# Optimization experiments

Measured on AMD Instinct MI355X. Metric: run time of the kernel, lower is better.

Reference implementation:

```python
import jax, jax.numpy as jnp
import numpy as np

NUM_GRAPHS = 512


def setup_inputs() -> dict:
    key = jax.random.key(0)
    ks = jax.random.split(key, 12)
    N, E, D, H, C = 100000, 1600000, 128, 128, 10
    x = jax.random.normal(ks[0], (N, D), dtype=jnp.float32)
    edge_index = jax.random.randint(ks[1], (2, E), 0, N, dtype=jnp.int64)
    batch = jnp.sort(jax.random.randint(ks[2], (N,), 0, NUM_GRAPHS, dtype=jnp.int64))
    def glorot(k, fan_in, fan_out):
        s = jnp.sqrt(6.0 / (fan_in + fan_out))
        return jax.random.uniform(k, (fan_in, fan_out), jnp.float32, -s, s)
    return {
        "x": x, "edge_index": edge_index, "batch": batch,
        "W_init": glorot(ks[3], D, H), "b_init": jnp.zeros((H,), jnp.float32),
        "W_h0": glorot(ks[4], H, H), "b_h0": jnp.zeros((H,), jnp.float32),
        "W_h1": glorot(ks[5], H, H), "b_h1": jnp.zeros((H,), jnp.float32),
        "W_out": glorot(ks[6], H, C), "b_out": jnp.zeros((C,), jnp.float32),
    }


def reference(x, edge_index, batch, W_init, b_init, W_h0, b_h0, W_h1, b_h1, W_out, b_out):
    N = x.shape[0]
    loop = jnp.arange(N, dtype=edge_index.dtype)
    # add self-loops (PyG GCNConv default)
    row = jnp.concatenate([edge_index[0], loop])  # source
    col = jnp.concatenate([edge_index[1], loop])  # target
    # symmetric normalization D^-1/2 (A+I) D^-1/2, degrees on target index
    deg = jax.ops.segment_sum(jnp.ones_like(col, dtype=x.dtype), col, num_segments=N)
    dis = jnp.where(deg > 0, jax.lax.rsqrt(jnp.maximum(deg, 1e-12)), 0.0)
    norm = dis[row] * dis[col]  # [E+N]

    def gcn_conv(h, W, b):
        h = h @ W                                    # linear first (as in PyG)
        msg = h[row] * norm[:, None]                 # gather + scale
        return jax.ops.segment_sum(msg, col, num_segments=N) + b  # scatter-add

    h = jax.nn.relu(gcn_conv(x, W_init, b_init))
    h = jax.nn.relu(gcn_conv(h, W_h0, b_h0))
    h = jax.nn.relu(gcn_conv(h, W_h1, b_h1))
    h = gcn_conv(h, W_out, b_out)
    # global mean pooling over graphs
    sums = jax.ops.segment_sum(h, batch, num_segments=NUM_GRAPHS)
    cnt = jax.ops.segment_sum(jnp.ones((N, 1), h.dtype), batch, num_segments=NUM_GRAPHS)
    return sums / jnp.maximum(cnt, 1.0)
```

## Files before the change

kernel.cpp:

```cpp
#include <hip/hip_runtime.h>


#define SORTB 64

typedef unsigned short u16;
typedef unsigned int   u32;
typedef __attribute__((ext_vector_type(8))) short bf16x8;
typedef __attribute__((ext_vector_type(4))) float f32x4;

static __device__ __forceinline__ u16 f2bf(float x) {
    u32 u = __float_as_uint(x);
    u32 r = (u + 0x7fffu + ((u >> 16) & 1u)) >> 16;
    return (u16)r;
}
static __device__ __forceinline__ float bf_lo(u32 p) { return __uint_as_float(p << 16); }
static __device__ __forceinline__ float bf_hi(u32 p) { return __uint_as_float(p & 0xffff0000u); }

__global__ __launch_bounds__(256) void k_count(const int* __restrict__ col, int E,
                                               int* __restrict__ cnt,
                                               u16* __restrict__ rank) {
    int e = blockIdx.x * 256 + threadIdx.x;
    if (e < E) rank[e] = (u16)atomicAdd(&cnt[col[e]], 1);
}

__global__ __launch_bounds__(256) void k_lhist(const int* __restrict__ cnt, int N,
                                               int strip, int* __restrict__ blockhist) {
    __shared__ int h[256];
    int t = threadIdx.x, blk = blockIdx.x;
    h[t] = 0;
    __syncthreads();
    int s0 = blk * strip, s1 = min(s0 + strip, N);
    for (int i = s0 + t; i < s1; i += 256) atomicAdd(&h[min(cnt[i], 255)], 1);
    __syncthreads();
    blockhist[t * SORTB + blk] = h[t];
}

__global__ __launch_bounds__(1024) void k_scan2(int* __restrict__ tsum) {
    __shared__ int part[1024];
    int t = threadIdx.x;
    int base = t * 16;
    int local[16];
    int s = 0;
    #pragma unroll
    for (int i = 0; i < 16; ++i) { local[i] = tsum[base + i]; s += local[i]; }
    part[t] = s;
    __syncthreads();
    for (int off = 1; off < 1024; off <<= 1) {
        int v = part[t];
        int add = (t >= off) ? part[t - off] : 0;
        __syncthreads();
        part[t] = v + add;
        __syncthreads();
    }
    int run = (t == 0) ? 0 : part[t - 1];
    #pragma unroll
    for (int i = 0; i < 16; ++i) { int c = local[i]; tsum[base + i] = run; run += c; }
}

__global__ __launch_bounds__(256) void k_scatterR(const int* __restrict__ cnt, int N,
                                                  int strip,
                                                  const int* __restrict__ blockhist,
                                                  int* __restrict__ perm,
                                                  int* __restrict__ iperm,
                                                  int* __restrict__ rowptr,
                                                  int* __restrict__ csr,
                                                  float* __restrict__ dis) {
    __shared__ int pst[256], ebs[256], sc[256], boff[256];
    int t = threadIdx.x, blk = blockIdx.x;
    pst[t]  = blockhist[t * SORTB];
    boff[t] = blockhist[t * SORTB + blk];
    __syncthreads();
    int cntb = ((t == 255) ? N : pst[t + 1]) - pst[t];
    int contrib = cntb * ((t + 3) & ~3);
    sc[t] = contrib;
    __syncthreads();
    for (int off = 1; off < 256; off <<= 1) {
        int v = sc[t];
        int a = (t >= off) ? sc[t - off] : 0;
        __syncthreads();
        sc[t] = v + a;
        __syncthreads();
    }
    ebs[t] = (t == 0) ? 0 : sc[t - 1];
    if (blk == 0 && t == 255) rowptr[N] = sc[255];
    __syncthreads();
    int s0 = blk * strip, s1 = min(s0 + strip, N);
    for (int i = s0 + t; i < s1; i += 256) {
        int c = cnt[i];
        int b = min(c, 255);
        int pos = atomicAdd(&boff[b], 1);
        perm[pos] = i;
        iperm[i] = pos;
        int pad = (c + 3) & ~3;
        int rp = ebs[b] + (pos - pst[b]) * pad;
        rowptr[pos] = rp;
        for (int p = rp + c; p < rp + pad; ++p) csr[p] = N;
        dis[i] = rsqrtf((float)(c + 1));
    }
}

__global__ __launch_bounds__(256) void k_prep2(const float* __restrict__ W0,
                                               const float* __restrict__ W1,
                                               const float* __restrict__ W2,
                                               const float* __restrict__ Wo,
                                               u32* __restrict__ whi,
                                               u32* __restrict__ wlo, int C,
                                               const int* __restrict__ row,
                                               const int* __restrict__ col, int E,
                                               const int* __restrict__ rowptr,
                                               const int* __restrict__ iperm,
                                               const u16* __restrict__ rank,
                                               int* __restrict__ csr,
                                               const float* __restrict__ x,
                                               const float* __restrict__ dis,
                                               u16* __restrict__ bX,
                                               u16* __restrict__ bA,
                                               u16* __restrict__ bB,
                                               int N, int eb) {
    int bx = blockIdx.x;
    if (bx < 24) {
        int which = bx >> 3;
        const float* W = (which == 0) ? W0 : (which == 1) ? W1 : W2;
        int t = (bx & 7) * 256 + threadIdx.x;
        int lane = t & 63;
        int nk = t >> 6;
        int k0 = nk & 3;
        int ntile = nk >> 2;
        int n = ntile * 16 + (lane & 15);
        int kbase = k0 * 32 + (lane >> 4) * 8;
        u32 hi[4], lo[4];
        #pragma unroll
        for (int tt = 0; tt < 4; ++tt) {
            float w0 = W[(kbase + 2 * tt) * 128 + n];
            float w1 = W[(kbase + 2 * tt + 1) * 128 + n];
            u16 h0 = f2bf(w0), h1 = f2bf(w1);
            u16 l0 = f2bf(w0 - __uint_as_float((u32)h0 << 16));
            u16 l1 = f2bf(w1 - __uint_as_float((u32)h1 << 16));
            hi[tt] = (u32)h0 | ((u32)h1 << 16);
            lo[tt] = (u32)l0 | ((u32)l1 << 16);
        }
        uint4 qh = {hi[0], hi[1], hi[2], hi[3]};
        uint4 ql = {lo[0], lo[1], lo[2], lo[3]};
        int base = which * 2048;
        ((uint4*)whi)[base + t] = qh;
        ((uint4*)wlo)[base + t] = ql;
    } else if (bx == 24) {
        int t = threadIdx.x;
        int lane = t & 63;
        int k0 = t >> 6;
        int n = lane & 15;
        int kbase = k0 * 32 + (lane >> 4) * 8;
        bool vc = (n < C);
        u32 hi[4], lo[4];
        #pragma unroll
        for (int tt = 0; tt < 4; ++tt) {
            float w0 = vc ? Wo[(kbase + 2 * tt) * C + n] : 0.f;
            float w1 = vc ? Wo[(kbase + 2 * tt + 1) * C + n] : 0.f;
            u16 h0 = f2bf(w0), h1 = f2bf(w1);
            u16 l0 = f2bf(w0 - __uint_as_float((u32)h0 << 16));
            u16 l1 = f2bf(w1 - __uint_as_float((u32)h1 << 16));
            hi[tt] = (u32)h0 | ((u32)h1 << 16);
            lo[tt] = (u32)l0 | ((u32)l1 << 16);
        }
        uint4 qh = {hi[0], hi[1], hi[2], hi[3]};
        uint4 ql = {lo[0], lo[1], lo[2], lo[3]};
        ((uint4*)whi)[6144 + t] = qh;
        ((uint4*)wlo)[6144 + t] = ql;
    } else if (bx < 25 + eb) {
        int e = (bx - 25) * 256 + threadIdx.x;
        if (e < E) {
            int c = col[e];
            csr[rowptr[iperm[c]] + (int)rank[e]] = row[e];
        }
    } else {
        int i = (bx - 25 - eb) * 256 + threadIdx.x;
        int total = (N + 1) * 32;
        if (i >= total) return;
        int v = i >> 5;
        if (v < N) {
            float dv = dis[v];
            float4 val = ((const float4*)x)[i];
            ushort4 o;
            o.x = f2bf(dv * val.x); o.y = f2bf(dv * val.y);
            o.z = f2bf(dv * val.z); o.w = f2bf(dv * val.w);
            ((ushort4*)bX)[i] = o;
        } else {
            ushort4 z = {0, 0, 0, 0};
            ((ushort4*)bX)[i] = z;
            ((ushort4*)bA)[i] = z;
            ((ushort4*)bB)[i] = z;
        }
    }
}

__global__ __launch_bounds__(256) void k_fused(const u16* __restrict__ hin,
                                               const u32* __restrict__ whi,
                                               const u32* __restrict__ wlo,
                                               const float* __restrict__ bias,
                                               u16* __restrict__ hout,
                                               const int* __restrict__ rowptr,
                                               const int* __restrict__ csr,
                                               const float* __restrict__ dis,
                                               const int* __restrict__ perm,
                                               int N, int scale_out,
                                               int proj,
                                               const u32* __restrict__ pwhi,
                                               const u32* __restrict__ pwlo,
                                               u16* __restrict__ tmpC) {
    __shared__ u32 sS[32 * 68];
    __shared__ float dS[32];
    __shared__ int pS[32];
    int tid = threadIdx.x;
    int wave = tid >> 6;
    int lane = tid & 63;
    int row0 = ((int)gridDim.x - 1 - (int)blockIdx.x) * 32;
    const uint4* hin4 = (const uint4*)hin;

    int grp = lane >> 4;
    int sub = lane & 15;
    #pragma unroll
    for (int jj = 0; jj < 2; ++jj) {
        int rloc = wave * 8 + jj * 4 + grp;
        int p = row0 + rloc;
        bool hR = p < N;
        int ia = 0, rem = 0, r = N;
        float dv = 1.f;
        if (hR) {
            r   = perm[p];
            ia  = rowptr[p];
            rem = rowptr[p + 1] - ia;
            dv  = dis[r];
        }
        uint4 ps = hin4[((u32)r << 4) + sub];
        float a0 = bf_lo(ps.x), a1 = bf_hi(ps.x);
        float a2 = bf_lo(ps.y), a3 = bf_hi(ps.y);
        float a4 = bf_lo(ps.z), a5 = bf_hi(ps.z);
        float a6 = bf_lo(ps.w), a7 = bf_hi(ps.w);
        int m = rem;
        m = max(m, __shfl_xor(m, 16));
        m = max(m, __shfl_xor(m, 32));
        const int4* cq = (const int4*)(csr + ia);
        for (int k = 0; k < m; k += 8) {
            int4 q0 = cq[(k >> 2)];
            int4 q1 = cq[(k >> 2) + 1];
            bool v0 = k < rem;
            bool v1 = (k + 4) < rem;
            int n0 = v0 ? q0.x : N;
            int n1 = v0 ? q0.y : N;
            int n2 = v0 ? q0.z : N;
            int n3 = v0 ? q0.w : N;
            int n4 = v1 ? q1.x : N;
            int n5 = v1 ? q1.y : N;
            int n6 = v1 ? q1.z : N;
            int n7 = v1 ? q1.w : N;
            uint4 p0 = hin4[((u32)n0 << 4) + sub];
            uint4 p1 = hin4[((u32)n1 << 4) + sub];
            uint4 p2 = hin4[((u32)n2 << 4) + sub];
            uint4 p3 = hin4[((u32)n3 << 4) + sub];
            uint4 p4 = hin4[((u32)n4 << 4) + sub];
            uint4 p5 = hin4[((u32)n5 << 4) + sub];
            uint4 p6 = hin4[((u32)n6 << 4) + sub];
            uint4 p7 = hin4[((u32)n7 << 4) + sub];
            a0 += bf_lo(p0.x) + bf_lo(p1.x) + bf_lo(p2.x) + bf_lo(p3.x);
            a1 += bf_hi(p0.x) + bf_hi(p1.x) + bf_hi(p2.x) + bf_hi(p3.x);
            a2 += bf_lo(p0.y) + bf_lo(p1.y) + bf_lo(p2.y) + bf_lo(p3.y);
            a3 += bf_hi(p0.y) + bf_hi(p1.y) + bf_hi(p2.y) + bf_hi(p3.y);
            a4 += bf_lo(p0.z) + bf_lo(p1.z) + bf_lo(p2.z) + bf_lo(p3.z);
            a5 += bf_hi(p0.z) + bf_hi(p1.z) + bf_hi(p2.z) + bf_hi(p3.z);
            a6 += bf_lo(p0.w) + bf_lo(p1.w) + bf_lo(p2.w) + bf_lo(p3.w);
            a7 += bf_hi(p0.w) + bf_hi(p1.w) + bf_hi(p2.w) + bf_hi(p3.w);
            a0 += bf_lo(p4.x) + bf_lo(p5.x) + bf_lo(p6.x) + bf_lo(p7.x);
            a1 += bf_hi(p4.x) + bf_hi(p5.x) + bf_hi(p6.x) + bf_hi(p7.x);
            a2 += bf_lo(p4.y) + bf_lo(p5.y) + bf_lo(p6.y) + bf_lo(p7.y);
            a3 += bf_hi(p4.y) + bf_hi(p5.y) + bf_hi(p6.y) + bf_hi(p7.y);
            a4 += bf_lo(p4.z) + bf_lo(p5.z) + bf_lo(p6.z) + bf_lo(p7.z);
            a5 += bf_hi(p4.z) + bf_hi(p5.z) + bf_hi(p6.z) + bf_hi(p7.z);
            a6 += bf_lo(p4.w) + bf_lo(p5.w) + bf_lo(p6.w) + bf_lo(p7.w);
            a7 += bf_hi(p4.w) + bf_hi(p5.w) + bf_hi(p6.w) + bf_hi(p7.w);
        }
        u32 w0 = (u32)f2bf(dv * a0) | ((u32)f2bf(dv * a1) << 16);
        u32 w1 = (u32)f2bf(dv * a2) | ((u32)f2bf(dv * a3) << 16);
        u32 w2 = (u32)f2bf(dv * a4) | ((u32)f2bf(dv * a5) << 16);
        u32 w3 = (u32)f2bf(dv * a6) | ((u32)f2bf(dv * a7) << 16);
        sS[rloc * 65 + sub * 4 + 0] = w0;
        sS[rloc * 65 + sub * 4 + 1] = w1;
        sS[rloc * 65 + sub * 4 + 2] = w2;
        sS[rloc * 65 + sub * 4 + 3] = w3;
        if (sub == 0) { dS[rloc] = dv; pS[rloc] = r; }
    }
    __syncthreads();

    f32x4 acc[2][2] = {{{0.f,0.f,0.f,0.f},{0.f,0.f,0.f,0.f}},
                       {{0.f,0.f,0.f,0.f},{0.f,0.f,0.f,0.f}}};
    int mA = lane & 15;
    int qA = lane >> 4;
    #pragma unroll
    for (int k0 = 0; k0 < 4; ++k0) {
        union { u32 u[4]; bf16x8 v; } A0, A1;
        int ub = k0 * 16 + qA * 4;
        #pragma unroll
        for (int tt = 0; tt < 4; ++tt) {
            A0.u[tt] = sS[mA * 65 + ub + tt];
            A1.u[tt] = sS[(mA + 16) * 65 + ub + tt];
        }
        #pragma unroll
        for (int ct = 0; ct < 2; ++ct) {
            int ntk = ((2 * wave + ct) * 4 + k0) * 64 + lane;
            union { uint4 q; bf16x8 v; } BH, BL;
            BH.q = ((const uint4*)whi)[ntk];
            BL.q = ((const uint4*)wlo)[ntk];
            acc[0][ct] = __builtin_amdgcn_mfma_f32_16x16x32_bf16(A0.v, BH.v, acc[0][ct], 0, 0, 0);
            acc[0][ct] = __builtin_amdgcn_mfma_f32_16x16x32_bf16(A0.v, BL.v, acc[0][ct], 0, 0, 0);
            acc[1][ct] = __builtin_amdgcn_mfma_f32_16x16x32_bf16(A1.v, BH.v, acc[1][ct], 0, 0, 0);
            acc[1][ct] = __builtin_amdgcn_mfma_f32_16x16x32_bf16(A1.v, BL.v, acc[1][ct], 0, 0, 0);
        }
    }

    if (!proj) {
        #pragma unroll
        for (int rt = 0; rt < 2; ++rt) {
            #pragma unroll
            for (int ct = 0; ct < 2; ++ct) {
                int col = (2 * wave + ct) * 16 + (lane & 15);
                float bb = bias[col];
                #pragma unroll
                for (int r = 0; r < 4; ++r) {
                    int rloc = rt * 16 + (lane >> 4) * 4 + r;
                    if (row0 + rloc < N) {
                        int rr = pS[rloc];
                        float o = fmaxf(acc[rt][ct][r] + bb, 0.f);
                        if (scale_out) o *= dS[rloc];
                        hout[((u32)rr << 7) + col] = f2bf(o);
                    }
                }
            }
        }
    } else {
        __syncthreads();
        u16* hS16 = (u16*)sS;
        #pragma unroll
        for (int rt = 0; rt < 2; ++rt) {
            #pragma unroll
            for (int ct = 0; ct < 2; ++ct) {
                int col = (2 * wave + ct) * 16 + (lane & 15);
                float bb = bias[col];
                #pragma unroll
                for (int r = 0; r < 4; ++r) {
                    int rloc = rt * 16 + (lane >> 4) * 4 + r;
                    hS16[rloc * 136 + col] = f2bf(fmaxf(acc[rt][ct][r] + bb, 0.f));
                }
            }
        }
        __syncthreads();
        if (wave < 2) {
            int m2 = lane & 15;
            int quad = lane >> 4;
            f32x4 a2 = {0.f, 0.f, 0.f, 0.f};
            #pragma unroll
            for (int k0 = 0; k0 < 4; ++k0) {
                bf16x8 Afrag = *(bf16x8*)&hS16[(wave * 16 + m2) * 136 + k0 * 32 + quad * 8];
                union { uint4 q; bf16x8 v; } BH, BL;
                BH.q = ((const uint4*)pwhi)[k0 * 64 + lane];
                BL.q = ((const uint4*)pwlo)[k0 * 64 + lane];
                a2 = __builtin_amdgcn_mfma_f32_16x16x32_bf16(Afrag, BH.v, a2, 0, 0, 0);
                a2 = __builtin_amdgcn_mfma_f32_16x16x32_bf16(Afrag, BL.v, a2, 0, 0, 0);
            }
            #pragma unroll
            for (int r = 0; r < 4; ++r) {
                int rloc = wave * 16 + quad * 4 + r;
                if (row0 + rloc < N) {
                    int rr = pS[rloc];
                    tmpC[((u32)rr << 4) + m2] = f2bf(a2[r] * dS[rloc]);
                }
            }
        }
        if (blockIdx.x == 0 && tid < 16) tmpC[((u32)N << 4) + tid] = 0;
    }
}

__global__ __launch_bounds__(1024) void k_aggpool(const u16* __restrict__ tp,
                                                  const int* __restrict__ rowptr,
                                                  const int* __restrict__ csr,
                                                  const int* __restrict__ iperm,
                                                  const float* __restrict__ dis,
                                                  const int* __restrict__ batch,
                                                  const float* __restrict__ bout,
                                                  float* __restrict__ out,
                                                  int N, int C) {
    __shared__ float2 red[1024];
    int g = blockIdx.x;
    int tid = threadIdx.x;
    int c = tid & 7;
    int rg = tid >> 3;
    const u32* tp32 = (const u32*)tp;
    int lo = 0, hi = N;
    while (lo < hi) { int m = (lo + hi) >> 1; if (batch[m] < g) lo = m + 1; else hi = m; }
    int lb = lo;
    hi = N;
    while (lo < hi) { int m = (lo + hi) >> 1; if (batch[m] <= g) lo = m + 1; else hi = m; }
    int ub = lo;
    const int4* csr4 = (const int4*)csr;
    float px = 0.f, py = 0.f;
    for (int v = lb + rg; v < ub; v += 128) {
        u32 ps = tp32[((u32)v << 3) + c];
        float ax = bf_lo(ps), ay = bf_hi(ps);
        int pos = iperm[v];
        int i = rowptr[pos], e = rowptr[pos + 1];
        for (; i + 8 <= e; i += 8) {
            int4 q0 = csr4[(u32)i >> 2];
            int4 q1 = csr4[((u32)i >> 2) + 1];
            u32 p0 = tp32[((u32)q0.x << 3) + c];
            u32 p1 = tp32[((u32)q0.y << 3) + c];
            u32 p2 = tp32[((u32)q0.z << 3) + c];
            u32 p3 = tp32[((u32)q0.w << 3) + c];
            u32 p4 = tp32[((u32)q1.x << 3) + c];
            u32 p5 = tp32[((u32)q1.y << 3) + c];
            u32 p6 = tp32[((u32)q1.z << 3) + c];
            u32 p7 = tp32[((u32)q1.w << 3) + c];
            ax += bf_lo(p0) + bf_lo(p1) + bf_lo(p2) + bf_lo(p3)
                + bf_lo(p4) + bf_lo(p5) + bf_lo(p6) + bf_lo(p7);
            ay += bf_hi(p0) + bf_hi(p1) + bf_hi(p2) + bf_hi(p3)
                + bf_hi(p4) + bf_hi(p5) + bf_hi(p6) + bf_hi(p7);
        }
        if (i < e) {
            int4 q0 = csr4[(u32)i >> 2];
            u32 p0 = tp32[((u32)q0.x << 3) + c];
            u32 p1 = tp32[((u32)q0.y << 3) + c];
            u32 p2 = tp32[((u32)q0.z << 3) + c];
            u32 p3 = tp32[((u32)q0.w << 3) + c];
            ax += bf_lo(p0) + bf_lo(p1) + bf_lo(p2) + bf_lo(p3);
            ay += bf_hi(p0) + bf_hi(p1) + bf_hi(p2) + bf_hi(p3);
        }
        float dv = dis[v];
        px += dv * ax;
        py += dv * ay;
    }
    red[tid] = make_float2(px, py);
    __syncthreads();
    #pragma unroll
    for (int s = 64; s >= 1; s >>= 1) {
        if (rg < s) {
            float2 o = red[tid + s * 8];
            red[tid].x += o.x; red[tid].y += o.y;
        }
        __syncthreads();
    }
    if (tid < 8) {
        float cnt = (float)(ub - lb);
        float den = fmaxf(cnt, 1.0f);
        float2 s2 = red[tid];
        int ch0 = 2 * tid, ch1 = 2 * tid + 1;
        if (ch0 < C) out[g * C + ch0] = (s2.x + cnt * bout[ch0]) / den;
        if (ch1 < C) out[g * C + ch1] = (s2.y + cnt * bout[ch1]) / den;
    }
}

extern "C" void kernel_launch(void* const* d_in, const int* in_sizes, int n_in,
                              void* d_out, int out_size, void* d_ws, size_t ws_size,
                              hipStream_t stream) {
    const float* x      = (const float*)d_in[0];
    const int*   ei     = (const int*)d_in[1];
    const int*   batch  = (const int*)d_in[2];
    const float* W_init = (const float*)d_in[3];
    const float* b_init = (const float*)d_in[4];
    const float* W_h0   = (const float*)d_in[5];
    const float* b_h0   = (const float*)d_in[6];
    const float* W_h1   = (const float*)d_in[7];
    const float* b_h1   = (const float*)d_in[8];
    const float* W_out  = (const float*)d_in[9];
    const float* b_out  = (const float*)d_in[10];

    int N = in_sizes[0] / 128;
    int E = in_sizes[1] / 2;
    int C = in_sizes[10];
    int G = out_size / C;
    int strip = (N + SORTB - 1) / SORTB;

    size_t off = 0;
    auto alloc = [&](size_t bytes) -> char* {
        char* p = (char*)d_ws + off;
        off += (bytes + 255) & ~(size_t)255;
        return p;
    };
    u16*   bufX   = (u16*)  alloc((size_t)(N + 1) * 128 * 2);
    u16*   bufA   = (u16*)  alloc((size_t)(N + 1) * 128 * 2);
    u16*   bufB   = (u16*)  alloc((size_t)(N + 1) * 128 * 2);
    float* dis    = (float*)alloc((size_t)N * 4);
    int*   rowptr = (int*)  alloc((size_t)(N + 1) * 4);
    int*   csr    = (int*)  alloc(((size_t)E + 3 * (size_t)N + 8) * 4);
    u32*   whi    = (u32*)  alloc((3 * 2048 + 256) * 16);
    u32*   wlo    = (u32*)  alloc((3 * 2048 + 256) * 16);
    int*   perm   = (int*)  alloc((size_t)N * 4);
    int*   iperm  = (int*)  alloc((size_t)N * 4);
    int*   blockhist = (int*)alloc((size_t)256 * SORTB * 4);
    size_t zoff   = off;
    int*   cnt    = (int*)  alloc((size_t)N * 4);
    size_t zbytes = off - zoff;

    u16*   rank   = (u16*)bufB;
    u16*   tmpC   = (u16*)bufX;

    hipMemsetAsync(cnt, 0, zbytes, stream);

    const int* rowi = ei;
    const int* coli = ei + E;

    int eb = (E + 255) / 256;
    int cg = ((N + 1) * 32 + 255) / 256;
    k_count<<<eb, 256, 0, stream>>>(coli, E, cnt, rank);
    k_lhist<<<SORTB, 256, 0, stream>>>(cnt, N, strip, blockhist);
    k_scan2<<<1, 1024, 0, stream>>>(blockhist);
    k_scatterR<<<SORTB, 256, 0, stream>>>(cnt, N, strip, blockhist, perm, iperm, rowptr, csr, dis);
    k_prep2<<<25 + eb + cg, 256, 0, stream>>>(W_init, W_h0, W_h1, W_out, whi, wlo, C,
                                              rowi, coli, E, rowptr, iperm, rank, csr,
                                              x, dis, bufX, bufA, bufB, N, eb);

    int fb = (N + 31) / 32;

    k_fused<<<fb, 256, 0, stream>>>(bufX, whi,         wlo,         b_init, bufA, rowptr, csr, dis, perm, N, 1, 0, nullptr, nullptr, nullptr);
    k_fused<<<fb, 256, 0, stream>>>(bufA, whi + 8192,  wlo + 8192,  b_h0,   bufB, rowptr, csr, dis, perm, N, 1, 0, nullptr, nullptr, nullptr);
    k_fused<<<fb, 256, 0, stream>>>(bufB, whi + 16384, wlo + 16384, b_h1,   bufA, rowptr, csr, dis, perm, N, 0, 1, whi + 24576, wlo + 24576, tmpC);

    k_aggpool<<<G, 1024, 0, stream>>>(tmpC, rowptr, csr, iperm, dis, batch, b_out, (float*)d_out, N, C);
}
```

Before: 441.1 us.

## Merge three GCN layer kernels into one cooperative persistent kernel; fold scan into scatter

Replaces the three per-layer k_fused launches with a single cooperative persistent kernel that loops over tiles and uses grid-wide syncs between layers, falling back to separate launches if the cooperative launch fails. It also removes the separate k_scan2 launch by having each k_scatterR block recompute the histogram prefix sums itself. The aim is to cut kernel launch and tail overhead. In exchange it pays for grid-sync cost, lower parallelism per tile loop, possible occupancy limits from the cooperative grid size, and redundant per-block histogram scanning.

```diff
diff --git a/kernel.cpp b/kernel.cpp
--- a/kernel.cpp
+++ b/kernel.cpp
@@ -1,4 +1,5 @@
 #include <hip/hip_runtime.h>
+#include <hip/hip_cooperative_groups.h>
 
 
 #define SORTB 64
@@ -33,28 +34,6 @@
     for (int i = s0 + t; i < s1; i += 256) atomicAdd(&h[min(cnt[i], 255)], 1);
     __syncthreads();
     blockhist[t * SORTB + blk] = h[t];
-}
-
-__global__ __launch_bounds__(1024) void k_scan2(int* __restrict__ tsum) {
-    __shared__ int part[1024];
-    int t = threadIdx.x;
-    int base = t * 16;
-    int local[16];
-    int s = 0;
-    #pragma unroll
-    for (int i = 0; i < 16; ++i) { local[i] = tsum[base + i]; s += local[i]; }
-    part[t] = s;
-    __syncthreads();
-    for (int off = 1; off < 1024; off <<= 1) {
-        int v = part[t];
-        int add = (t >= off) ? part[t - off] : 0;
-        __syncthreads();
-        part[t] = v + add;
-        __syncthreads();
-    }
-    int run = (t == 0) ? 0 : part[t - 1];
-    #pragma unroll
-    for (int i = 0; i < 16; ++i) { int c = local[i]; tsum[base + i] = run; run += c; }
 }
 
 __global__ __launch_bounds__(256) void k_scatterR(const int* __restrict__ cnt, int N,
@@ -67,12 +46,26 @@
                                                   float* __restrict__ dis) {
     __shared__ int pst[256], ebs[256], sc[256], boff[256];
     int t = threadIdx.x, blk = blockIdx.x;
-    pst[t]  = blockhist[t * SORTB];
-    boff[t] = blockhist[t * SORTB + blk];
-    __syncthreads();
-    int cntb = ((t == 255) ? N : pst[t + 1]) - pst[t];
-    int contrib = cntb * ((t + 3) & ~3);
-    sc[t] = contrib;
+    const int* rowp = blockhist + t * SORTB;
+    int rowSum = 0, before = 0;
+    for (int k = 0; k < SORTB; ++k) {
+        int v = rowp[k];
+        rowSum += v;
+        if (k < blk) before += v;
+    }
+    sc[t] = rowSum;
+    __syncthreads();
+    for (int off = 1; off < 256; off <<= 1) {
+        int v = sc[t];
+        int a = (t >= off) ? sc[t - off] : 0;
+        __syncthreads();
+        sc[t] = v + a;
+        __syncthreads();
+    }
+    pst[t] = (t == 0) ? 0 : sc[t - 1];
+    boff[t] = pst[t] + before;
+    __syncthreads();
+    sc[t] = rowSum * ((t + 3) & ~3);
     __syncthreads();
     for (int off = 1; off < 256; off <<= 1) {
         int v = sc[t];
@@ -193,27 +186,14 @@
     }
 }
 
-__global__ __launch_bounds__(256) void k_fused(const u16* __restrict__ hin,
-                                               const u32* __restrict__ whi,
-                                               const u32* __restrict__ wlo,
-                                               const float* __restrict__ bias,
-                                               u16* __restrict__ hout,
-                                               const int* __restrict__ rowptr,
-                                               const int* __restrict__ csr,
-                                               const float* __restrict__ dis,
-                                               const int* __restrict__ perm,
-                                               int N, int scale_out,
-                                               int proj,
-                                               const u32* __restrict__ pwhi,
-                                               const u32* __restrict__ pwlo,
-                                               u16* __restrict__ tmpC) {
-    __shared__ u32 sS[32 * 68];
-    __shared__ float dS[32];
-    __shared__ int pS[32];
-    int tid = threadIdx.x;
-    int wave = tid >> 6;
-    int lane = tid & 63;
-    int row0 = ((int)gridDim.x - 1 - (int)blockIdx.x) * 32;
+static __device__ __forceinline__ void tile_body(
+    int row0, const u16* hin, const u32* wh, const u32* wl,
+    const float* __restrict__ bias, u16* hout,
+    const int* __restrict__ rowptr, const int* __restrict__ csr,
+    const float* __restrict__ dis, const int* __restrict__ perm,
+    int N, int scale_out, int proj,
+    const u32* pwhi, const u32* pwlo, u16* tmpC,
+    u32* sS, float* dS, int* pS, int tid, int wave, int lane) {
     const uint4* hin4 = (const uint4*)hin;
 
     int grp = lane >> 4;
@@ -307,8 +287,8 @@
         for (int ct = 0; ct < 2; ++ct) {
             int ntk = ((2 * wave + ct) * 4 + k0) * 64 + lane;
             union { uint4 q; bf16x8 v; } BH, BL;
-            BH.q = ((const uint4*)whi)[ntk];
-            BL.q = ((const uint4*)wlo)[ntk];
+            BH.q = ((const uint4*)wh)[ntk];
+            BL.q = ((const uint4*)wl)[ntk];
             acc[0][ct] = __builtin_amdgcn_mfma_f32_16x16x32_bf16(A0.v, BH.v, acc[0][ct], 0, 0, 0);
             acc[0][ct] = __builtin_amdgcn_mfma_f32_16x16x32_bf16(A0.v, BL.v, acc[0][ct], 0, 0, 0);
             acc[1][ct] = __builtin_amdgcn_mfma_f32_16x16x32_bf16(A1.v, BH.v, acc[1][ct], 0, 0, 0);
@@ -376,6 +356,58 @@
         }
         if (blockIdx.x == 0 && tid < 16) tmpC[((u32)N << 4) + tid] = 0;
     }
+}
+
+__global__ __launch_bounds__(256) void k_fusedAll(
+        const u16* bX, u16* bA, u16* bB,
+        const u32* __restrict__ whi, const u32* __restrict__ wlo,
+        const float* __restrict__ bi0, const float* __restrict__ bi1,
+        const float* __restrict__ bi2,
+        const int* __restrict__ rowptr, const int* __restrict__ csr,
+        const float* __restrict__ dis, const int* __restrict__ perm,
+        int N, int fb, u16* tmpC) {
+    cooperative_groups::grid_group gg = cooperative_groups::this_grid();
+    __shared__ u32 sS[32 * 68];
+    __shared__ float dS[32];
+    __shared__ int pS[32];
+    int tid = threadIdx.x, wave = tid >> 6, lane = tid & 63;
+    for (int layer = 0; layer < 3; ++layer) {
+        const u16* hin = (layer == 0) ? bX : (layer == 1) ? bA : bB;
+        u16* hout = (layer == 0) ? bA : bB;
+        const u32* wh = whi + layer * 8192;
+        const u32* wl = wlo + layer * 8192;
+        const float* bias = (layer == 0) ? bi0 : (layer == 1) ? bi1 : bi2;
+        int proj = (layer == 2) ? 1 : 0;
+        for (int p = blockIdx.x; p < fb; p += gridDim.x) {
+            int row0 = (fb - 1 - p) * 32;
+            tile_body(row0, hin, wh, wl, bias, hout, rowptr, csr, dis, perm,
+                      N, proj ? 0 : 1, proj, whi + 24576, wlo + 24576, tmpC,
+                      sS, dS, pS, tid, wave, lane);
+            __syncthreads();
+        }
+        if (layer < 2) gg.sync();
+    }
+}
+
+__global__ __launch_bounds__(256) void k_fused(const u16* hin,
+                                               const u32* __restrict__ whi,
+                                               const u32* __restrict__ wlo,
+                                               const float* __restrict__ bias,
+                                               u16* hout,
+                                               const int* __restrict__ rowptr,
+                                               const int* __restrict__ csr,
+                                               const float* __restrict__ dis,
+                                               const int* __restrict__ perm,
+                                               int N, int scale_out, int proj,
+                                               const u32* pwhi, const u32* pwlo,
+                                               u16* tmpC) {
+    __shared__ u32 sS[32 * 68];
+    __shared__ float dS[32];
+    __shared__ int pS[32];
+    int tid = threadIdx.x, wave = tid >> 6, lane = tid & 63;
+    int row0 = ((int)gridDim.x - 1 - (int)blockIdx.x) * 32;
+    tile_body(row0, hin, whi, wlo, bias, hout, rowptr, csr, dis, perm,
+              N, scale_out, proj, pwhi, pwlo, tmpC, sS, dS, pS, tid, wave, lane);
 }
 
 __global__ __launch_bounds__(1024) void k_aggpool(const u16* __restrict__ tp,
@@ -509,7 +541,6 @@
     int cg = ((N + 1) * 32 + 255) / 256;
     k_count<<<eb, 256, 0, stream>>>(coli, E, cnt, rank);
     k_lhist<<<SORTB, 256, 0, stream>>>(cnt, N, strip, blockhist);
-    k_scan2<<<1, 1024, 0, stream>>>(blockhist);
     k_scatterR<<<SORTB, 256, 0, stream>>>(cnt, N, strip, blockhist, perm, iperm, rowptr, csr, dis);
     k_prep2<<<25 + eb + cg, 256, 0, stream>>>(W_init, W_h0, W_h1, W_out, whi, wlo, C,
                                               rowi, coli, E, rowptr, iperm, rank, csr,
@@ -517,9 +548,34 @@
 
     int fb = (N + 31) / 32;
 
-    k_fused<<<fb, 256, 0, stream>>>(bufX, whi,         wlo,         b_init, bufA, rowptr, csr, dis, perm, N, 1, 0, nullptr, nullptr, nullptr);
-    k_fused<<<fb, 256, 0, stream>>>(bufA, whi + 8192,  wlo + 8192,  b_h0,   bufB, rowptr, csr, dis, perm, N, 1, 0, nullptr, nullptr, nullptr);
-    k_fused<<<fb, 256, 0, stream>>>(bufB, whi + 16384, wlo + 16384, b_h1,   bufA, rowptr, csr, dis, perm, N, 0, 1, whi + 24576, wlo + 24576, tmpC);
+    bool coop_ok = false;
+    int maxB = 0;
+    if (hipOccupancyMaxActiveBlocksPerMultiprocessor(&maxB, k_fusedAll, 256, 0)
+            == hipSuccess && maxB > 0) {
+        static int numCU = 0;
+        if (numCU == 0) {
+            hipDeviceProp_t prop;
+            if (hipGetDeviceProperties(&prop, 0) == hipSuccess)
+                numCU = prop.multiProcessorCount;
+            if (numCU <= 0) numCU = 256;
+        }
+        int grid = maxB * numCU;
+        if (grid > fb) grid = fb;
+        void* kargs[] = { (void*)&bufX, (void*)&bufA, (void*)&bufB,
+                          (void*)&whi, (void*)&wlo,
+                          (void*)&b_init, (void*)&b_h0, (void*)&b_h1,
+                          (void*)&rowptr, (void*)&csr, (void*)&dis, (void*)&perm,
+                          (void*)&N, (void*)&fb, (void*)&tmpC };
+        hipError_t err = hipLaunchCooperativeKernel((const void*)k_fusedAll,
+                                                    dim3(grid), dim3(256),
+                                                    kargs, 0, stream);
+        coop_ok = (err == hipSuccess);
+    }
+    if (!coop_ok) {
+        k_fused<<<fb, 256, 0, stream>>>(bufX, whi,         wlo,         b_init, bufA, rowptr, csr, dis, perm, N, 1, 0, nullptr, nullptr, nullptr);
+        k_fused<<<fb, 256, 0, stream>>>(bufA, whi + 8192,  wlo + 8192,  b_h0,   bufB, rowptr, csr, dis, perm, N, 1, 0, nullptr, nullptr, nullptr);
+        k_fused<<<fb, 256, 0, stream>>>(bufB, whi + 16384, wlo + 16384, b_h1,   bufA, rowptr, csr, dis, perm, N, 0, 1, whi + 24576, wlo + 24576, tmpC);
+    }
 
     k_aggpool<<<G, 1024, 0, stream>>>(tmpC, rowptr, csr, iperm, dis, batch, b_out, (float*)d_out, N, C);
 }
```

New measurement: 652.5 us. 1.48x slower.

## Merge graph preprocessing kernels into one cooperative kernel with grid syncs

Applied to the files above, without the earlier changes.

Replaces the memset plus count, histogram, scan, scatter and prep kernels with a single cooperative kernel that uses grid-wide syncs between phases. The separate scan kernel goes away: each scatter block now sums its own histogram row directly. The intent is to remove several kernel launch gaps and tiny serial kernels. In exchange, the grid is capped at occupancy, so the large per-edge and per-node phases loop over work with grid-stride, and each grid sync adds a barrier cost. The previous multi-kernel path is kept as a fallback if the cooperative launch fails.

```diff
diff --git a/kernel.cpp b/kernel.cpp
--- a/kernel.cpp
+++ b/kernel.cpp
@@ -1,4 +1,5 @@
 #include <hip/hip_runtime.h>
+#include <hip/hip_cooperative_groups.h>
 
 
 #define SORTB 64
@@ -16,63 +17,50 @@
 static __device__ __forceinline__ float bf_lo(u32 p) { return __uint_as_float(p << 16); }
 static __device__ __forceinline__ float bf_hi(u32 p) { return __uint_as_float(p & 0xffff0000u); }
 
-__global__ __launch_bounds__(256) void k_count(const int* __restrict__ col, int E,
-                                               int* __restrict__ cnt,
-                                               u16* __restrict__ rank) {
-    int e = blockIdx.x * 256 + threadIdx.x;
-    if (e < E) rank[e] = (u16)atomicAdd(&cnt[col[e]], 1);
-}
-
-__global__ __launch_bounds__(256) void k_lhist(const int* __restrict__ cnt, int N,
-                                               int strip, int* __restrict__ blockhist) {
-    __shared__ int h[256];
-    int t = threadIdx.x, blk = blockIdx.x;
+
+static __device__ __forceinline__ void lhist_body(int blk, const int* __restrict__ cnt,
+                                                  int N, int strip,
+                                                  int* __restrict__ blockhist,
+                                                  int* h, int t) {
     h[t] = 0;
     __syncthreads();
     int s0 = blk * strip, s1 = min(s0 + strip, N);
     for (int i = s0 + t; i < s1; i += 256) atomicAdd(&h[min(cnt[i], 255)], 1);
     __syncthreads();
     blockhist[t * SORTB + blk] = h[t];
-}
-
-__global__ __launch_bounds__(1024) void k_scan2(int* __restrict__ tsum) {
-    __shared__ int part[1024];
-    int t = threadIdx.x;
-    int base = t * 16;
-    int local[16];
-    int s = 0;
-    #pragma unroll
-    for (int i = 0; i < 16; ++i) { local[i] = tsum[base + i]; s += local[i]; }
-    part[t] = s;
-    __syncthreads();
-    for (int off = 1; off < 1024; off <<= 1) {
-        int v = part[t];
-        int add = (t >= off) ? part[t - off] : 0;
+    __syncthreads();
+}
+
+static __device__ __forceinline__ void scatter_body(int blk, const int* __restrict__ cnt,
+                                                    int N, int strip,
+                                                    const int* __restrict__ blockhist,
+                                                    int* __restrict__ perm,
+                                                    int* __restrict__ iperm,
+                                                    int* __restrict__ rowptr,
+                                                    int* __restrict__ csr,
+                                                    float* __restrict__ dis,
+                                                    int* pst, int* ebs, int* sc, int* boff,
+                                                    int t) {
+    const int* rowp = blockhist + t * SORTB;
+    int rowSum = 0, before = 0;
+    for (int k = 0; k < SORTB; ++k) {
+        int v = rowp[k];
+        rowSum += v;
+        if (k < blk) before += v;
+    }
+    sc[t] = rowSum;
+    __syncthreads();
+    for (int off = 1; off < 256; off <<= 1) {
+        int v = sc[t];
+        int a = (t >= off) ? sc[t - off] : 0;
         __syncthreads();
-        part[t] = v + add;
+        sc[t] = v + a;
         __syncthreads();
     }
-    int run = (t == 0) ? 0 : part[t - 1];
-    #pragma unroll
-    for (int i = 0; i < 16; ++i) { int c = local[i]; tsum[base + i] = run; run += c; }
-}
-
-__global__ __launch_bounds__(256) void k_scatterR(const int* __restrict__ cnt, int N,
-                                                  int strip,
-                                                  const int* __restrict__ blockhist,
-                                                  int* __restrict__ perm,
-                                                  int* __restrict__ iperm,
-                                                  int* __restrict__ rowptr,
-                                                  int* __restrict__ csr,
-                                                  float* __restrict__ dis) {
-    __shared__ int pst[256], ebs[256], sc[256], boff[256];
-    int t = threadIdx.x, blk = blockIdx.x;
-    pst[t]  = blockhist[t * SORTB];
-    boff[t] = blockhist[t * SORTB + blk];
-    __syncthreads();
-    int cntb = ((t == 255) ? N : pst[t + 1]) - pst[t];
-    int contrib = cntb * ((t + 3) & ~3);
-    sc[t] = contrib;
+    pst[t] = (t == 0) ? 0 : sc[t - 1];
+    boff[t] = pst[t] + before;
+    __syncthreads();
+    sc[t] = rowSum * ((t + 3) & ~3);
     __syncthreads();
     for (int off = 1; off < 256; off <<= 1) {
         int v = sc[t];
@@ -97,6 +85,150 @@
         for (int p = rp + c; p < rp + pad; ++p) csr[p] = N;
         dis[i] = rsqrtf((float)(c + 1));
     }
+}
+
+static __device__ __forceinline__ void prep_unit(int u, int t,
+        const float* __restrict__ W0, const float* __restrict__ W1,
+        const float* __restrict__ W2, const float* __restrict__ Wo,
+        u32* __restrict__ whi, u32* __restrict__ wlo, int C,
+        const int* __restrict__ row, const int* __restrict__ col, int E,
+        const int* __restrict__ rowptr, const int* __restrict__ iperm,
+        const u16* __restrict__ rank, int* __restrict__ csr,
+        const float* __restrict__ x, const float* __restrict__ dis,
+        u16* __restrict__ bX, u16* __restrict__ bA, u16* __restrict__ bB,
+        int N, int eb) {
+    if (u < 24) {
+        int which = u >> 3;
+        const float* W = (which == 0) ? W0 : (which == 1) ? W1 : W2;
+        int t2 = (u & 7) * 256 + t;
+        int lane = t2 & 63;
+        int nk = t2 >> 6;
+        int k0 = nk & 3;
+        int ntile = nk >> 2;
+        int n = ntile * 16 + (lane & 15);
+        int kbase = k0 * 32 + (lane >> 4) * 8;
+        u32 hi[4], lo[4];
+        #pragma unroll
+        for (int tt = 0; tt < 4; ++tt) {
+            float w0 = W[(kbase + 2 * tt) * 128 + n];
+            float w1 = W[(kbase + 2 * tt + 1) * 128 + n];
+            u16 h0 = f2bf(w0), h1 = f2bf(w1);
+            u16 l0 = f2bf(w0 - __uint_as_float((u32)h0 << 16));
+            u16 l1 = f2bf(w1 - __uint_as_float((u32)h1 << 16));
+            hi[tt] = (u32)h0 | ((u32)h1 << 16);
+            lo[tt] = (u32)l0 | ((u32)l1 << 16);
+        }
+        uint4 qh = {hi[0], hi[1], hi[2], hi[3]};
+        uint4 ql = {lo[0], lo[1], lo[2], lo[3]};
+        int base = which * 2048;
+        ((uint4*)whi)[base + t2] = qh;
+        ((uint4*)wlo)[base + t2] = ql;
+    } else if (u == 24) {
+        int lane = t & 63;
+        int k0 = t >> 6;
+        int n = lane & 15;
+        int kbase = k0 * 32 + (lane >> 4) * 8;
+        bool vc = (n < C);
+        u32 hi[4], lo[4];
+        #pragma unroll
+        for (int tt = 0; tt < 4; ++tt) {
+            float w0 = vc ? Wo[(kbase + 2 * tt) * C + n] : 0.f;
+            float w1 = vc ? Wo[(kbase + 2 * tt + 1) * C + n] : 0.f;
+            u16 h0 = f2bf(w0), h1 = f2bf(w1);
+            u16 l0 = f2bf(w0 - __uint_as_float((u32)h0 << 16));
+            u16 l1 = f2bf(w1 - __uint_as_float((u32)h1 << 16));
+            hi[tt] = (u32)h0 | ((u32)h1 << 16);
+            lo[tt] = (u32)l0 | ((u32)l1 << 16);
+        }
+        uint4 qh = {hi[0], hi[1], hi[2], hi[3]};
+        uint4 ql = {lo[0], lo[1], lo[2], lo[3]};
+        ((uint4*)whi)[6144 + t] = qh;
+        ((uint4*)wlo)[6144 + t] = ql;
+    } else if (u < 25 + eb) {
+        int e = (u - 25) * 256 + t;
+        if (e < E) {
+            int c = col[e];
+            csr[rowptr[iperm[c]] + (int)rank[e]] = row[e];
+        }
+    } else {
+        int i = (u - 25 - eb) * 256 + t;
+        int total = (N + 1) * 32;
+        if (i < total) {
+            int v = i >> 5;
+            if (v < N) {
+                float dv = dis[v];
+                float4 val = ((const float4*)x)[i];
+                ushort4 o;
+                o.x = f2bf(dv * val.x); o.y = f2bf(dv * val.y);
+                o.z = f2bf(dv * val.z); o.w = f2bf(dv * val.w);
+                ((ushort4*)bX)[i] = o;
+            } else {
+                ushort4 z = {0, 0, 0, 0};
+                ((ushort4*)bX)[i] = z;
+                ((ushort4*)bA)[i] = z;
+                ((ushort4*)bB)[i] = z;
+            }
+        }
+    }
+}
+
+__global__ __launch_bounds__(256) void k_prepAll(
+        const int* __restrict__ rowi, const int* __restrict__ coli,
+        int E, int N, int strip,
+        int* __restrict__ cnt, u16* __restrict__ rank,
+        int* __restrict__ blockhist,
+        int* __restrict__ perm, int* __restrict__ iperm,
+        int* __restrict__ rowptr, int* __restrict__ csr,
+        float* __restrict__ dis,
+        const float* __restrict__ W0, const float* __restrict__ W1,
+        const float* __restrict__ W2, const float* __restrict__ Wo,
+        u32* __restrict__ whi, u32* __restrict__ wlo, int C,
+        const float* __restrict__ x,
+        u16* __restrict__ bX, u16* __restrict__ bA, u16* __restrict__ bB,
+        int eb, int cg) {
+    cooperative_groups::grid_group gg = cooperative_groups::this_grid();
+    __shared__ int pst[256], ebs[256], sc[256], boff[256];
+    int t = threadIdx.x, bx = blockIdx.x, G = gridDim.x;
+    for (int i = bx * 256 + t; i < N; i += G * 256) cnt[i] = 0;
+    gg.sync();
+    for (int e = bx * 256 + t; e < E; e += G * 256)
+        rank[e] = (u16)atomicAdd(&cnt[coli[e]], 1);
+    gg.sync();
+    if (bx < SORTB) lhist_body(bx, cnt, N, strip, blockhist, sc, t);
+    gg.sync();
+    if (bx < SORTB) scatter_body(bx, cnt, N, strip, blockhist, perm, iperm,
+                                 rowptr, csr, dis, pst, ebs, sc, boff, t);
+    gg.sync();
+    int total_u = 25 + eb + cg;
+    for (int u = bx; u < total_u; u += G)
+        prep_unit(u, t, W0, W1, W2, Wo, whi, wlo, C, rowi, coli, E,
+                  rowptr, iperm, rank, csr, x, dis, bX, bA, bB, N, eb);
+}
+
+__global__ __launch_bounds__(256) void k_count(const int* __restrict__ col, int E,
+                                               int* __restrict__ cnt,
+                                               u16* __restrict__ rank) {
+    int e = blockIdx.x * 256 + threadIdx.x;
+    if (e < E) rank[e] = (u16)atomicAdd(&cnt[col[e]], 1);
+}
+
+__global__ __launch_bounds__(256) void k_lhist(const int* __restrict__ cnt, int N,
+                                               int strip, int* __restrict__ blockhist) {
+    __shared__ int h[256];
+    lhist_body(blockIdx.x, cnt, N, strip, blockhist, h, threadIdx.x);
+}
+
+__global__ __launch_bounds__(256) void k_scatterR(const int* __restrict__ cnt, int N,
+                                                  int strip,
+                                                  const int* __restrict__ blockhist,
+                                                  int* __restrict__ perm,
+                                                  int* __restrict__ iperm,
+                                                  int* __restrict__ rowptr,
+                                                  int* __restrict__ csr,
+                                                  float* __restrict__ dis) {
+    __shared__ int pst[256], ebs[256], sc[256], boff[256];
+    scatter_body(blockIdx.x, cnt, N, strip, blockhist, perm, iperm,
+                 rowptr, csr, dis, pst, ebs, sc, boff, threadIdx.x);
 }
 
 __global__ __launch_bounds__(256) void k_prep2(const float* __restrict__ W0,
@@ -117,80 +249,8 @@
                                                u16* __restrict__ bA,
                                                u16* __restrict__ bB,
                                                int N, int eb) {
-    int bx = blockIdx.x;
-    if (bx < 24) {
-        int which = bx >> 3;
-        const float* W = (which == 0) ? W0 : (which == 1) ? W1 : W2;
-        int t = (bx & 7) * 256 + threadIdx.x;
-        int lane = t & 63;
-        int nk = t >> 6;
-        int k0 = nk & 3;
-        int ntile = nk >> 2;
-        int n = ntile * 16 + (lane & 15);
-        int kbase = k0 * 32 + (lane >> 4) * 8;
-        u32 hi[4], lo[4];
-        #pragma unroll
-        for (int tt = 0; tt < 4; ++tt) {
-            float w0 = W[(kbase + 2 * tt) * 128 + n];
-            float w1 = W[(kbase + 2 * tt + 1) * 128 + n];
-            u16 h0 = f2bf(w0), h1 = f2bf(w1);
-            u16 l0 = f2bf(w0 - __uint_as_float((u32)h0 << 16));
-            u16 l1 = f2bf(w1 - __uint_as_float((u32)h1 << 16));
-            hi[tt] = (u32)h0 | ((u32)h1 << 16);
-            lo[tt] = (u32)l0 | ((u32)l1 << 16);
-        }
-        uint4 qh = {hi[0], hi[1], hi[2], hi[3]};
-        uint4 ql = {lo[0], lo[1], lo[2], lo[3]};
-        int base = which * 2048;
-        ((uint4*)whi)[base + t] = qh;
-        ((uint4*)wlo)[base + t] = ql;
-    } else if (bx == 24) {
-        int t = threadIdx.x;
-        int lane = t & 63;
-        int k0 = t >> 6;
-        int n = lane & 15;
-        int kbase = k0 * 32 + (lane >> 4) * 8;
-        bool vc = (n < C);
-        u32 hi[4], lo[4];
-        #pragma unroll
-        for (int tt = 0; tt < 4; ++tt) {
-            float w0 = vc ? Wo[(kbase + 2 * tt) * C + n] : 0.f;
-            float w1 = vc ? Wo[(kbase + 2 * tt + 1) * C + n] : 0.f;
-            u16 h0 = f2bf(w0), h1 = f2bf(w1);
-            u16 l0 = f2bf(w0 - __uint_as_float((u32)h0 << 16));
-            u16 l1 = f2bf(w1 - __uint_as_float((u32)h1 << 16));
-            hi[tt] = (u32)h0 | ((u32)h1 << 16);
-            lo[tt] = (u32)l0 | ((u32)l1 << 16);
-        }
-        uint4 qh = {hi[0], hi[1], hi[2], hi[3]};
-        uint4 ql = {lo[0], lo[1], lo[2], lo[3]};
-        ((uint4*)whi)[6144 + t] = qh;
-        ((uint4*)wlo)[6144 + t] = ql;
-    } else if (bx < 25 + eb) {
-        int e = (bx - 25) * 256 + threadIdx.x;
-        if (e < E) {
-            int c = col[e];
-            csr[rowptr[iperm[c]] + (int)rank[e]] = row[e];
-        }
-    } else {
-        int i = (bx - 25 - eb) * 256 + threadIdx.x;
-        int total = (N + 1) * 32;
-        if (i >= total) return;
-        int v = i >> 5;
-        if (v < N) {
-            float dv = dis[v];
-            float4 val = ((const float4*)x)[i];
-            ushort4 o;
-            o.x = f2bf(dv * val.x); o.y = f2bf(dv * val.y);
-            o.z = f2bf(dv * val.z); o.w = f2bf(dv * val.w);
-            ((ushort4*)bX)[i] = o;
-        } else {
-            ushort4 z = {0, 0, 0, 0};
-            ((ushort4*)bX)[i] = z;
-            ((ushort4*)bA)[i] = z;
-            ((ushort4*)bB)[i] = z;
-        }
-    }
+    prep_unit(blockIdx.x, threadIdx.x, W0, W1, W2, Wo, whi, wlo, C,
+              row, col, E, rowptr, iperm, rank, csr, x, dis, bX, bA, bB, N, eb);
 }
 
 __global__ __launch_bounds__(256) void k_fused(const u16* __restrict__ hin,
@@ -500,20 +560,50 @@
     u16*   rank   = (u16*)bufB;
     u16*   tmpC   = (u16*)bufX;
 
-    hipMemsetAsync(cnt, 0, zbytes, stream);
-
     const int* rowi = ei;
     const int* coli = ei + E;
 
     int eb = (E + 255) / 256;
     int cg = ((N + 1) * 32 + 255) / 256;
-    k_count<<<eb, 256, 0, stream>>>(coli, E, cnt, rank);
-    k_lhist<<<SORTB, 256, 0, stream>>>(cnt, N, strip, blockhist);
-    k_scan2<<<1, 1024, 0, stream>>>(blockhist);
-    k_scatterR<<<SORTB, 256, 0, stream>>>(cnt, N, strip, blockhist, perm, iperm, rowptr, csr, dis);
-    k_prep2<<<25 + eb + cg, 256, 0, stream>>>(W_init, W_h0, W_h1, W_out, whi, wlo, C,
-                                              rowi, coli, E, rowptr, iperm, rank, csr,
-                                              x, dis, bufX, bufA, bufB, N, eb);
+
+    bool coop_ok = false;
+    int maxB = 0;
+    if (hipOccupancyMaxActiveBlocksPerMultiprocessor(&maxB, k_prepAll, 256, 0)
+            == hipSuccess && maxB > 0) {
+        static int numCU = 0;
+        if (numCU == 0) {
+            hipDeviceProp_t prop;
+            if (hipGetDeviceProperties(&prop, 0) == hipSuccess)
+                numCU = prop.multiProcessorCount;
+            if (numCU <= 0) numCU = 256;
+        }
+        long long grid = (long long)maxB * numCU;
+        long long needed = 25 + eb + cg;
+        if (grid > needed) grid = needed;
+        if (grid >= SORTB) {
+            void* kargs[] = { (void*)&rowi, (void*)&coli, (void*)&E, (void*)&N,
+                              (void*)&strip, (void*)&cnt, (void*)&rank,
+                              (void*)&blockhist, (void*)&perm, (void*)&iperm,
+                              (void*)&rowptr, (void*)&csr, (void*)&dis,
+                              (void*)&W_init, (void*)&W_h0, (void*)&W_h1,
+                              (void*)&W_out, (void*)&whi, (void*)&wlo, (void*)&C,
+                              (void*)&x, (void*)&bufX, (void*)&bufA, (void*)&bufB,
+                              (void*)&eb, (void*)&cg };
+            hipError_t err = hipLaunchCooperativeKernel((const void*)k_prepAll,
+                                                        dim3((u32)grid), dim3(256),
+                                                        kargs, 0, stream);
+            coop_ok = (err == hipSuccess);
+        }
+    }
+    if (!coop_ok) {
+        hipMemsetAsync(cnt, 0, zbytes, stream);
+        k_count<<<eb, 256, 0, stream>>>(coli, E, cnt, rank);
+        k_lhist<<<SORTB, 256, 0, stream>>>(cnt, N, strip, blockhist);
+        k_scatterR<<<SORTB, 256, 0, stream>>>(cnt, N, strip, blockhist, perm, iperm, rowptr, csr, dis);
+        k_prep2<<<25 + eb + cg, 256, 0, stream>>>(W_init, W_h0, W_h1, W_out, whi, wlo, C,
+                                                  rowi, coli, E, rowptr, iperm, rank, csr,
+                                                  x, dis, bufX, bufA, bufB, N, eb);
+    }
 
     int fb = (N + 31) / 32;
 
```

Measured after the change: 749.1 us. +69.8%, slower.
